# Performance work log

Measured on AMD Instinct MI355X. Metric: run time of the kernel, lower is better.

The kernel has to match this reference:

```python
import jax, jax.numpy as jnp
import numpy as np
from jax import lax

B, CIN, CV, H, W = 2, 256, 128, 96, 320
NS, K, PAD = 8, 3, 1
HID = 4 * CV
EPS = 1e-5

def _ffn_shapes(p):
    return {p+'_g': (CV,), p+'_b': (CV,), p+'_w1': (CV, HID), p+'_b1': (HID,),
            p+'_dw': (HID, 1, 3, 3), p+'_bdw': (HID,), p+'_w2': (HID, CV), p+'_b2': (CV,)}

def _win_shapes(p):
    return {p+'_g': (CV,), p+'_b': (CV,), p+'_wq': (CV, CV), p+'_wk': (CV, CV),
            p+'_wv': (CV, CV), p+'_wo': (CV, CV), p+'_bo': (CV,)}

PARAM_SHAPES = {'agg_w1': (CIN, CIN // 2), 'agg_b1': (CIN // 2,), 'agg_w2': (CIN // 2, CV), 'agg_b2': (CV,),
                'ol_g': (CV,), 'ol_b': (CV,), 'ol_wv': (CV, CV), 'ol_wa': (CV, K ** 4), 'ol_ba': (K ** 4,),
                'ol_wo': (CV, CV), 'ol_bo': (CV,)}
PARAM_SHAPES.update(_ffn_shapes('f1')); PARAM_SHAPES.update(_win_shapes('w'))
PARAM_SHAPES.update(_ffn_shapes('f2')); PARAM_SHAPES.update(_win_shapes('s'))
PARAM_SHAPES.update(_ffn_shapes('f3'))
PNAMES = list(PARAM_SHAPES.keys())


def ln(x, g, b):
    mu = x.mean(-1, keepdims=True)
    var = ((x - mu) ** 2).mean(-1, keepdims=True)
    return (x - mu) * lax.rsqrt(var + EPS) * g + b


def sink_softmax(logits):
    # softmax with an implicit extra zero-logit 'sink' slot (sink competition):
    # probs = exp(l) / (sum(exp(l)) + exp(0)), computed stably.
    m = jnp.maximum(logits.max(-1, keepdims=True), 0.0)
    e = jnp.exp(logits - m)
    return e / (e.sum(-1, keepdims=True) + jnp.exp(-m))


def outlook_attn(x, g, b, wv, wa, ba, wo, bo):
    # VOLO-style outlook attention, kernel K, stride 1, padding PAD (pool is identity at stride 1)
    Bb, Hh, Ww, C = x.shape
    xn = ln(x, g, b)
    v = xn @ wv                                                     # B,H,W,C
    vp = jnp.pad(v, ((0, 0), (PAD, PAD), (PAD, PAD), (0, 0)))
    patches = jnp.stack([vp[:, i:i + Hh, j:j + Ww, :] for i in range(K) for j in range(K)], axis=3)  # B,H,W,K*K,C
    attn = (xn @ wa + ba).reshape(Bb, Hh, Ww, K * K, K * K)
    attn = sink_softmax(attn)
    out = jnp.einsum('bhwpq,bhwqc->bhwpc', attn, patches)           # B,H,W,K*K,C
    acc = jnp.zeros_like(vp)                                        # fold (overlap-add)
    idx = 0
    for i in range(K):
        for j in range(K):
            acc = acc.at[:, i:i + Hh, j:j + Ww, :].add(out[:, :, :, idx, :])
            idx += 1
    y = acc[:, PAD:PAD + Hh, PAD:PAD + Ww, :]
    return y @ wo + bo


def swin_mask(Hh, Ww, wh, ww):
    # standard swin shifted-window cross-region mask, built statically
    sh, sw = wh // 2, ww // 2
    img = np.zeros((Hh, Ww), np.int32)
    cnt = 0
    for hs in (slice(0, -wh), slice(-wh, -sh), slice(-sh, None)):
        for ws in (slice(0, -ww), slice(-ww, -sw), slice(-sw, None)):
            img[hs, ws] = cnt; cnt += 1
    win = img.reshape(Hh // wh, wh, Ww // ww, ww).transpose(0, 2, 1, 3).reshape(-1, wh * ww)
    mask = np.where(win[:, :, None] != win[:, None, :], -100.0, 0.0).astype(np.float32)
    return jnp.asarray(mask)  # [NS*NS, L, L]


def window_attn(x, g, b, wq, wk, wv, wo, bo, with_shift):
    Bb, Hh, Ww, C = x.shape
    wh, ww = Hh // NS, Ww // NS
    xn = ln(x, g, b)
    if with_shift:
        xn = jnp.roll(xn, (-(wh // 2), -(ww // 2)), axis=(1, 2))

    def part(t):  # -> [B, NS*NS, wh*ww, C]
        return t.reshape(Bb, NS, wh, NS, ww, C).transpose(0, 1, 3, 2, 4, 5).reshape(Bb, NS * NS, wh * ww, C)

    q, k, v = part(xn @ wq), part(xn @ wk), part(xn @ wv)
    scores = jnp.einsum('bnqc,bnkc->bnqk', q, k) / jnp.sqrt(jnp.asarray(C, x.dtype))
    if with_shift:
        scores = scores + swin_mask(Hh, Ww, wh, ww)[None]
    out = jnp.einsum('bnqk,bnkc->bnqc', sink_softmax(scores), v)
    out = out.reshape(Bb, NS, NS, wh, ww, C).transpose(0, 1, 3, 2, 4, 5).reshape(Bb, Hh, Ww, C)
    if with_shift:
        out = jnp.roll(out, (wh // 2, ww // 2), axis=(1, 2))
    return out @ wo + bo


def conv_ffn(x, g, b, w1, b1, dw, bdw, w2, b2):
    # pre-norm conv FFN: 1x1 expand -> depthwise 3x3 -> GELU -> 1x1 project
    xn = ln(x, g, b)
    h = (xn @ w1 + b1).transpose(0, 3, 1, 2)                        # B,HID,H,W
    h = lax.conv_general_dilated(h, dw, (1, 1), 'SAME', feature_group_count=HID)
    h = h + bdw[None, :, None, None]
    h = jax.nn.gelu(h, approximate=False).transpose(0, 2, 3, 1)
    return h @ w2 + b2


def pos_embed(Bb, Hh, Ww, nf, dtype):
    # DETR-style normalized 2D sine/cosine positional embedding, nf feats per axis
    scale = 2.0 * np.pi
    eps = 1e-6
    ye = jnp.arange(1, Hh + 1, dtype=jnp.float32); ye = ye / (ye[-1] + eps) * scale
    xe = jnp.arange(1, Ww + 1, dtype=jnp.float32); xe = xe / (xe[-1] + eps) * scale
    dim_t = 10000.0 ** (2.0 * (jnp.arange(nf) // 2) / nf)

    def emb(p):  # [N] -> [N, nf]
        t = p[:, None] / dim_t
        return jnp.stack([jnp.sin(t[:, 0::2]), jnp.cos(t[:, 1::2])], axis=2).reshape(p.shape[0], -1)

    py, px = emb(ye), emb(xe)
    pos = jnp.concatenate([jnp.broadcast_to(py[:, None, :], (Hh, Ww, nf)),
                           jnp.broadcast_to(px[None, :, :], (Hh, Ww, nf))], axis=-1)
    return jnp.broadcast_to(pos[None], (Bb, Hh, Ww, 2 * nf)).astype(dtype)


def forward(x, p):
    f = x.transpose(0, 2, 3, 1)                                     # B,H,W,CIN
    f = jax.nn.relu(f @ p['agg_w1'] + p['agg_b1'])                  # channels_agg (BN folded, eval)
    f = f @ p['agg_w2'] + p['agg_b2']                               # B,H,W,CV
    f = f + outlook_attn(f, p['ol_g'], p['ol_b'], p['ol_wv'], p['ol_wa'], p['ol_ba'], p['ol_wo'], p['ol_bo'])
    f = f + conv_ffn(f, p['f1_g'], p['f1_b'], p['f1_w1'], p['f1_b1'], p['f1_dw'], p['f1_bdw'], p['f1_w2'], p['f1_b2'])
    f = f + pos_embed(f.shape[0], f.shape[1], f.shape[2], CV // 2, f.dtype)
    f = f + window_attn(f, p['w_g'], p['w_b'], p['w_wq'], p['w_wk'], p['w_wv'], p['w_wo'], p['w_bo'], False)
    f = f + conv_ffn(f, p['f2_g'], p['f2_b'], p['f2_w1'], p['f2_b1'], p['f2_dw'], p['f2_bdw'], p['f2_w2'], p['f2_b2'])
    f = f + window_attn(f, p['s_g'], p['s_b'], p['s_wq'], p['s_wk'], p['s_wv'], p['s_wo'], p['s_bo'], True)
    f = f + conv_ffn(f, p['f3_g'], p['f3_b'], p['f3_w1'], p['f3_b1'], p['f3_dw'], p['f3_bdw'], p['f3_w2'], p['f3_b2'])
    return f.transpose(0, 3, 1, 2)                                  # B,CV,H,W


def setup_inputs():
    keys = iter(jax.random.split(jax.random.key(0), 64))
    inp = {'x': jax.random.normal(next(keys), (B, CIN, H, W), jnp.float32)}
    for name, shp in PARAM_SHAPES.items():
        if name.endswith('_g'):
            inp[name] = jnp.ones(shp, jnp.float32)
        elif len(shp) == 1:
            inp[name] = jnp.zeros(shp, jnp.float32)
        else:
            inp[name] = jax.random.normal(next(keys), shp, jnp.float32) * 0.02
    return inp


def reference(x, agg_w1, agg_b1, agg_w2, agg_b2, ol_g, ol_b, ol_wv, ol_wa, ol_ba, ol_wo, ol_bo,
              f1_g, f1_b, f1_w1, f1_b1, f1_dw, f1_bdw, f1_w2, f1_b2,
              w_g, w_b, w_wq, w_wk, w_wv, w_wo, w_bo,
              f2_g, f2_b, f2_w1, f2_b1, f2_dw, f2_bdw, f2_w2, f2_b2,
              s_g, s_b, s_wq, s_wk, s_wv, s_wo, s_bo,
              f3_g, f3_b, f3_w1, f3_b1, f3_dw, f3_bdw, f3_w2, f3_b2):
    _l = locals()
    p = {k: _l[k] for k in PNAMES}
    return forward(x, p)
```

## Files before the change

kernel.cpp:

```cpp
#include <hip/hip_runtime.h>

typedef __bf16 bf16;
typedef __bf16 bf16x8 __attribute__((ext_vector_type(8)));
typedef __bf16 bf16x4 __attribute__((ext_vector_type(4)));
typedef float  f32x4  __attribute__((ext_vector_type(4)));

#define MFMA_BF16(a, b, c) __builtin_amdgcn_mfma_f32_16x16x32_bf16(a, b, c, 0, 0, 0)

constexpr int cB    = 2;
constexpr int cH    = 96;
constexpr int cW    = 320;
constexpr int cC    = 128;
constexpr int cNPIX = cH * cW;
constexpr int cNTOK = cB * cNPIX;
constexpr int cAS   = 84;

struct WJob  { const float* src; bf16* dst; int K; int M; };
struct WJobs { WJob j[19]; };

__global__ __launch_bounds__(256) void k_wt(WJobs jobs)
{
    __shared__ float tile[32][33];
    const WJob jb = jobs.j[blockIdx.z];
    int k0 = blockIdx.y * 32, m0 = blockIdx.x * 32;
    if (k0 >= jb.K || m0 >= jb.M) return;
    int tx = threadIdx.x, ty = threadIdx.y;
#pragma unroll
    for (int i = 0; i < 32; i += 8) {
        int kk = k0 + ty + i, mm = m0 + tx;
        tile[ty + i][tx] = (kk < jb.K && mm < jb.M) ? jb.src[(size_t)kk * jb.M + mm] : 0.f;
    }
    __syncthreads();
#pragma unroll
    for (int i = 0; i < 32; i += 8) {
        int mm = m0 + ty + i, kk = k0 + tx;
        if (mm < jb.M && kk < jb.K)
            jb.dst[(size_t)mm * jb.K + kk] = (bf16)tile[tx][ty + i];
    }
}

__global__ __launch_bounds__(256) void k_dwt(const float* s0, const float* s1, const float* s2,
                                             float* d0, float* d1, float* d2)
{
    const float* s = blockIdx.x == 0 ? s0 : (blockIdx.x == 1 ? s1 : s2);
    float*       d = blockIdx.x == 0 ? d0 : (blockIdx.x == 1 ? d1 : d2);
    for (int i = threadIdx.x; i < 512 * 9; i += 256) {
        int c = i / 9, tap = i - c * 9;
        d[tap * 512 + c] = s[i];
    }
}

__global__ __launch_bounds__(256) void k_postab(float* __restrict__ yt, float* __restrict__ xt)
{
    int i = blockIdx.x * 256 + threadIdx.x;
    const float TWO_PI = 6.283185307179586f;
    const float KSC = -9.210340371976184f / 32.f;
    if (i < 96 * 64) {
        int h = i >> 6, c = i & 63;
        float p = (float)(h + 1) * (TWO_PI / (96.f + 1e-6f));
        float val = p * expf((float)(c >> 1) * KSC);
        yt[i] = (c & 1) ? cosf(val) : sinf(val);
    }
    if (i < 320 * 64) {
        int w = i >> 6, c = i & 63;
        float p = (float)(w + 1) * (TWO_PI / (320.f + 1e-6f));
        float val = p * expf((float)(c >> 1) * KSC);
        xt[i] = (c & 1) ? cosf(val) : sinf(val);
    }
}

__global__ __launch_bounds__(256) void k_chw2hwc(const float* __restrict__ in,
                                                 bf16* __restrict__ out)
{
    __shared__ float tile[32][33];
    const int Cc = 256;
    int s0 = blockIdx.x * 32;
    int c0 = blockIdx.y * 32;
    int b  = blockIdx.z;
    const float* ip = in  + (size_t)b * Cc * cNPIX;
    bf16*        op = out + (size_t)b * cNPIX * Cc;
    int tx = threadIdx.x, ty = threadIdx.y;
#pragma unroll
    for (int i = 0; i < 32; i += 8)
        tile[ty + i][tx] = ip[(size_t)(c0 + ty + i) * cNPIX + s0 + tx];
    __syncthreads();
#pragma unroll
    for (int i = 0; i < 32; i += 8)
        op[(size_t)(s0 + ty + i) * Cc + c0 + tx] = (bf16)tile[tx][ty + i];
}

__global__ __launch_bounds__(256) void k_hwc2chw(const float* __restrict__ in,
                                                 float* __restrict__ out)
{
    __shared__ float tile[32][33];
    int s0 = blockIdx.x * 32;
    int c0 = blockIdx.y * 32;
    int b  = blockIdx.z;
    const float* ip = in  + (size_t)b * cNPIX * cC;
    float*       op = out + (size_t)b * cC * cNPIX;
    int tx = threadIdx.x, ty = threadIdx.y;
#pragma unroll
    for (int i = 0; i < 32; i += 8)
        tile[ty + i][tx] = ip[(size_t)(s0 + ty + i) * cC + c0 + tx];
    __syncthreads();
#pragma unroll
    for (int i = 0; i < 32; i += 8)
        op[(size_t)(c0 + ty + i) * cNPIX + s0 + tx] = tile[tx][ty + i];
}

template<int QKVS>
__global__ __launch_bounds__(256) void k_gemm128(const bf16* __restrict__ A,
                                                 const bf16* __restrict__ Wt,
                                                 const float* __restrict__ bias,
                                                 bf16* __restrict__ outB, int M,
                                                 bf16* __restrict__ vtb,
                                                 bf16* __restrict__ ksb)
{
    __shared__ bf16 As[128][136];
    __shared__ bf16 Sb[64][136];

    const int NS = M >> 7;
    const int l  = blockIdx.x;
    const int r8 = l % (8 * NS);
    const int qq = l / (8 * NS);
    const int bm = (qq * 8 + (r8 & 7)) * 128;
    const int bn = (r8 >> 3) * 128;

    const int t = threadIdx.x;
    const int lane = t & 63, wid = t >> 6;
    const int wm = (wid >> 1) * 64, wn = (wid & 1) * 64;
    const int lr = lane & 15, lg = lane >> 4;

    const bf16* wp = Wt + (size_t)(bn + wn + lr) * 128 + lg * 8;
    bf16x8 bwA[4], bwB[4];
#pragma unroll
    for (int nf = 0; nf < 4; ++nf)
        bwA[nf] = *(const bf16x8*)(wp + (size_t)(nf * 16) * 128);

#pragma unroll
    for (int i = 0; i < 8; ++i) {
        int o = i * 256 + t;
        int row = o >> 4, cg = (o & 15) * 8;
        *(bf16x8*)&As[row][cg] = *(const bf16x8*)(A + (size_t)(bm + row) * 128 + cg);
    }
    __syncthreads();

    const f32x4 zero4 = {0.f, 0.f, 0.f, 0.f};
    f32x4 acc[4][4];
#pragma unroll
    for (int i = 0; i < 4; ++i)
#pragma unroll
        for (int j = 0; j < 4; ++j) acc[i][j] = zero4;

#pragma unroll
    for (int ks = 0; ks < 4; ++ks) {
        const bf16x8* cur = (ks & 1) ? bwB : bwA;
        bf16x8*       nxt = (ks & 1) ? bwA : bwB;
        if (ks < 3) {
#pragma unroll
            for (int nf = 0; nf < 4; ++nf)
                nxt[nf] = *(const bf16x8*)(wp + (size_t)(nf * 16) * 128 + (ks + 1) * 32);
        }
        bf16x8 af[4];
#pragma unroll
        for (int mf = 0; mf < 4; ++mf)
            af[mf] = *(const bf16x8*)&As[wm + mf*16 + lr][ks*32 + lg*8];
        __builtin_amdgcn_s_setprio(1);
#pragma unroll
        for (int mf = 0; mf < 4; ++mf)
#pragma unroll
            for (int nf = 0; nf < 4; ++nf)
                acc[mf][nf] = MFMA_BF16(af[mf], cur[nf], acc[mf][nf]);
        __builtin_amdgcn_s_setprio(0);
    }

    const bool vpart = (QKVS >= 0) && (bn == 256);
    const bool kpart = (QKVS >= 0) && (bn == 128);
    if (!vpart) {
#pragma unroll
        for (int half = 0; half < 2; ++half) {
            __syncthreads();
            if ((wid >> 1) == half) {
#pragma unroll
                for (int nf = 0; nf < 4; ++nf) {
                    int col = wn + nf * 16 + lr;
                    float bv = bias ? bias[bn + col] : 0.f;
#pragma unroll
                    for (int mf = 0; mf < 4; ++mf)
#pragma unroll
                        for (int r = 0; r < 4; ++r)
                            Sb[mf * 16 + lg * 4 + r][col] = (bf16)(acc[mf][nf][r] + bv);
                }
            }
            __syncthreads();
            if (!kpart) {
                const int ldo = (QKVS >= 0) ? 128 : M;
#pragma unroll
                for (int i = 0; i < 4; ++i) {
                    int o = i * 256 + t;
                    int row = o >> 4, cg = (o & 15) * 8;
                    *(bf16x8*)(outB + (size_t)(bm + half * 64 + row) * ldo + bn + cg) =
                        *(const bf16x8*)&Sb[row][cg];
                }
            } else {
#pragma unroll
                for (int i = 0; i < 4; ++i) {
                    int o = i * 256 + t;
                    int row = o >> 4, cg = (o & 15) * 8;
                    int gt = bm + half * 64 + row;
                    int b_ = gt / cNPIX, hw = gt - b_ * cNPIX;
                    int h = hw / cW, w = hw - (hw / cW) * cW;
                    int h0 = (QKVS == 1) ? ((h + 90) % 96)  : h;
                    int w0 = (QKVS == 1) ? ((w + 300) % 320) : w;
                    int nh = h0 / 12, kh = h0 - nh * 12;
                    int nw = w0 / 40, kw = w0 - nw * 40;
                    size_t krow = (size_t)((b_ * 64 + nh * 8 + nw) * 480 + kh * 40 + kw);
                    *(bf16x8*)(ksb + krow * 128 + cg) = *(const bf16x8*)&Sb[row][cg];
                }
            }
        }
    } else {
        const int lr_ = t & 15, cg_ = t >> 4;
        const int gt = bm + lr_ * 8;
        const int b_ = gt / cNPIX, hw = gt % cNPIX;
        const int h = hw / cW, w = hw % cW;
        const int h0 = (QKVS == 1) ? ((h + 90) % 96) : h;
        const int nh = h0 / 12, kh = h0 - nh * 12;
#pragma unroll
        for (int cp = 0; cp < 2; ++cp) {
            __syncthreads();
            if ((wid & 1) == cp) {
#pragma unroll
                for (int nf = 0; nf < 4; ++nf) {
                    int cl = nf * 16 + lr;
#pragma unroll
                    for (int mf = 0; mf < 4; ++mf)
#pragma unroll
                        for (int r = 0; r < 4; ++r)
                            Sb[cl][wm + mf * 16 + lg * 4 + r] = (bf16)acc[mf][nf][r];
                }
            }
            __syncthreads();
#pragma unroll
            for (int i = 0; i < 4; ++i) {
                int chl = cg_ + 16 * i;
                int ch  = cp * 64 + chl;
                bf16x8 e = *(const bf16x8*)&Sb[chl][lr_ * 8];
#pragma unroll
                for (int hi = 0; hi < 2; ++hi) {
                    int wv = (QKVS == 1) ? ((w + hi * 4 + 300) % 320) : (w + hi * 4);
                    int nw = wv / 40, kw = wv - nw * 40;
                    bf16* dst = vtb + ((size_t)((b_ * 64 + nh * 8 + nw) * 128 + ch)) * 480 + kh * 40 + kw;
                    bf16x4 hv;
#pragma unroll
                    for (int j = 0; j < 4; ++j) hv[j] = e[hi * 4 + j];
                    *(bf16x4*)dst = hv;
                }
            }
        }
    }
}

__global__ __launch_bounds__(256) void k_gemm128_wa(const bf16* __restrict__ A,
                                                    const bf16* __restrict__ Wt,
                                                    const float* __restrict__ bias,
                                                    bf16* __restrict__ outA)
{
    __shared__ bf16 As[128][136];
    __shared__ bf16 Sb[64][88];

    const int bm = blockIdx.x * 128;
    const int t = threadIdx.x;
    const int lane = t & 63, wid = t >> 6;
    const int wm = (wid >> 1) * 64, wn = (wid & 1) * 64;
    const int lr = lane & 15, lg = lane >> 4;

    bf16x8 zrow;
#pragma unroll
    for (int j = 0; j < 8; ++j) zrow[j] = (bf16)0.f;

    bool okc[4];
    const bf16* wp = Wt + (size_t)(wn + lr) * 128 + lg * 8;
#pragma unroll
    for (int nf = 0; nf < 4; ++nf) okc[nf] = (wn + nf * 16 + lr) < 81;

    bf16x8 bwA[4], bwB[4];
#pragma unroll
    for (int nf = 0; nf < 4; ++nf)
        bwA[nf] = okc[nf] ? *(const bf16x8*)(wp + (size_t)(nf * 16) * 128) : zrow;

#pragma unroll
    for (int i = 0; i < 8; ++i) {
        int o = i * 256 + t;
        int row = o >> 4, cg = (o & 15) * 8;
        *(bf16x8*)&As[row][cg] = *(const bf16x8*)(A + (size_t)(bm + row) * 128 + cg);
    }
    __syncthreads();

    const f32x4 zero4 = {0.f, 0.f, 0.f, 0.f};
    f32x4 acc[4][4];
#pragma unroll
    for (int i = 0; i < 4; ++i)
#pragma unroll
        for (int j = 0; j < 4; ++j) acc[i][j] = zero4;

#pragma unroll
    for (int ks = 0; ks < 4; ++ks) {
        const bf16x8* cur = (ks & 1) ? bwB : bwA;
        bf16x8*       nxt = (ks & 1) ? bwA : bwB;
        if (ks < 3) {
#pragma unroll
            for (int nf = 0; nf < 4; ++nf)
                nxt[nf] = okc[nf] ? *(const bf16x8*)(wp + (size_t)(nf * 16) * 128 + (ks + 1) * 32) : zrow;
        }
        bf16x8 af[4];
#pragma unroll
        for (int mf = 0; mf < 4; ++mf)
            af[mf] = *(const bf16x8*)&As[wm + mf*16 + lr][ks*32 + lg*8];
        __builtin_amdgcn_s_setprio(1);
#pragma unroll
        for (int mf = 0; mf < 4; ++mf)
#pragma unroll
            for (int nf = 0; nf < 4; ++nf)
                acc[mf][nf] = MFMA_BF16(af[mf], cur[nf], acc[mf][nf]);
        __builtin_amdgcn_s_setprio(0);
    }

#pragma unroll
    for (int half = 0; half < 2; ++half) {
        __syncthreads();
        if ((wid >> 1) == half) {
#pragma unroll
            for (int nf = 0; nf < 4; ++nf) {
                int col = wn + nf * 16 + lr;
                if (col >= 84) continue;
                float bv = (col < 81) ? bias[col] : 0.f;
#pragma unroll
                for (int mf = 0; mf < 4; ++mf)
#pragma unroll
                    for (int r = 0; r < 4; ++r) {
                        float vv = (col < 81) ? (acc[mf][nf][r] + bv) : 0.f;
                        Sb[mf * 16 + lg * 4 + r][col] = (bf16)vv;
                    }
            }
        }
        __syncthreads();
#pragma unroll
        for (int i = 0; i < 6; ++i) {
            int o = i * 256 + t;
            if (o < 64 * 21) {
                int row = o / 21, cq = (o - row * 21) * 4;
                *(bf16x4*)(outA + (size_t)(bm + half * 64 + row) * cAS + cq) =
                    *(const bf16x4*)&Sb[row][cq];
            }
        }
    }
}

template<bool OUTBF, bool RELU, bool RES, bool POS, bool LNOUT>
__global__ __launch_bounds__(256) void k_gemm_res(const bf16* __restrict__ A,
                                                  const bf16* __restrict__ Wt,
                                                  const float* __restrict__ bias,
                                                  const float* __restrict__ res,
                                                  float* __restrict__ outF,
                                                  bf16* __restrict__ outB,
                                                  int K,
                                                  const float* __restrict__ ytab,
                                                  const float* __restrict__ xtab,
                                                  const float* __restrict__ lng,
                                                  const float* __restrict__ lnb,
                                                  bf16* __restrict__ xnbO)
{
    __shared__ bf16 As[128][40];
    __shared__ bf16 Bs[128][40];
    __shared__ float Sf[64][136];

    const int bm = blockIdx.x * 128;
    const int t = threadIdx.x;
    const int lane = t & 63, wid = t >> 6;
    const int wm = (wid >> 1) * 64, wn = (wid & 1) * 64;
    const int lr = lane & 15, lg = lane >> 4;

    const f32x4 zero4 = {0.f, 0.f, 0.f, 0.f};
    f32x4 acc[4][4];
#pragma unroll
    for (int i = 0; i < 4; ++i)
#pragma unroll
        for (int j = 0; j < 4; ++j) acc[i][j] = zero4;

    for (int k0 = 0; k0 < K; k0 += 32) {
#pragma unroll
        for (int i = 0; i < 2; ++i) {
            int idx = t + i * 256;
            int row = idx >> 2, kg = (idx & 3) * 8;
            *(bf16x8*)&As[row][kg] = *(const bf16x8*)(A + (size_t)(bm + row) * K + k0 + kg);
            *(bf16x8*)&Bs[row][kg] = *(const bf16x8*)(Wt + (size_t)row * K + k0 + kg);
        }
        __syncthreads();
        bf16x8 af[4], bf[4];
#pragma unroll
        for (int mf = 0; mf < 4; ++mf)
            af[mf] = *(const bf16x8*)&As[wm + mf*16 + lr][lg * 8];
#pragma unroll
        for (int nf = 0; nf < 4; ++nf)
            bf[nf] = *(const bf16x8*)&Bs[wn + nf*16 + lr][lg * 8];
        __builtin_amdgcn_s_setprio(1);
#pragma unroll
        for (int mf = 0; mf < 4; ++mf)
#pragma unroll
            for (int nf = 0; nf < 4; ++nf)
                acc[mf][nf] = MFMA_BF16(af[mf], bf[nf], acc[mf][nf]);
        __builtin_amdgcn_s_setprio(0);
        __syncthreads();
    }

    if (OUTBF) {
        bf16 (*Sb)[136] = (bf16(*)[136])Sf;
#pragma unroll
        for (int nf = 0; nf < 4; ++nf) {
            int col = wn + nf * 16 + lr;
            float bv = bias ? bias[col] : 0.f;
#pragma unroll
            for (int mf = 0; mf < 4; ++mf)
#pragma unroll
                for (int r = 0; r < 4; ++r) {
                    float vv = acc[mf][nf][r] + bv;
                    if (RELU) vv = fmaxf(vv, 0.f);
                    Sb[wm + mf * 16 + lg * 4 + r][col] = (bf16)vv;
                }
        }
        __syncthreads();
#pragma unroll
        for (int i = 0; i < 8; ++i) {
            int o = i * 256 + t;
            int row = o >> 4, cg = (o & 15) * 8;
            *(bf16x8*)(outB + (size_t)(bm + row) * 128 + cg) = *(const bf16x8*)&Sb[row][cg];
        }
    } else {
        for (int half = 0; half < 2; ++half) {
            __syncthreads();
            if ((wid >> 1) == half) {
#pragma unroll
                for (int nf = 0; nf < 4; ++nf) {
                    int col = wn + nf * 16 + lr;
                    float bv = bias ? bias[col] : 0.f;
#pragma unroll
                    for (int mf = 0; mf < 4; ++mf)
#pragma unroll
                        for (int r = 0; r < 4; ++r)
                            Sf[mf * 16 + lg * 4 + r][col] = acc[mf][nf][r] + bv;
                }
            }
            __syncthreads();
#pragma unroll
            for (int i = 0; i < 8; ++i) {
                int o = i * 256 + t;
                int row = o >> 5, cq = (o & 31) * 4;
                int grow = bm + half * 64 + row;
                float4 v = *(const float4*)&Sf[row][cq];
                if (POS) {
                    int hw = grow % cNPIX;
                    int h = hw / cW, w = hw - (hw / cW) * cW;
                    float4 p = (cq < 64) ? *(const float4*)(ytab + (h << 6) + cq)
                                         : *(const float4*)(xtab + (w << 6) + cq - 64);
                    v.x += p.x; v.y += p.y; v.z += p.z; v.w += p.w;
                }
                if (RES) {
                    float4 rr = *(const float4*)(res + (size_t)grow * 128 + cq);
                    v.x += rr.x; v.y += rr.y; v.z += rr.z; v.w += rr.w;
                }
                if (LNOUT) {
                    float s  = v.x + v.y + v.z + v.w;
                    float sq = v.x*v.x + v.y*v.y + v.z*v.z + v.w*v.w;
#pragma unroll
                    for (int mk = 1; mk < 32; mk <<= 1) {
                        s  += __shfl_xor(s,  mk);
                        sq += __shfl_xor(sq, mk);
                    }
                    float mu = s * (1.f / 128.f);
                    float rs = rsqrtf(sq * (1.f / 128.f) - mu * mu + 1e-5f);
                    float4 g4 = *(const float4*)(lng + cq);
                    float4 b4 = *(const float4*)(lnb + cq);
                    bf16x4 xo;
                    xo[0] = (bf16)((v.x - mu) * rs * g4.x + b4.x);
                    xo[1] = (bf16)((v.y - mu) * rs * g4.y + b4.y);
                    xo[2] = (bf16)((v.z - mu) * rs * g4.z + b4.z);
                    xo[3] = (bf16)((v.w - mu) * rs * g4.w + b4.w);
                    *(bf16x4*)(xnbO + (size_t)grow * 128 + cq) = xo;
                }
                *(float4*)(outF + (size_t)grow * 128 + cq) = v;
            }
        }
    }
}

__global__ __launch_bounds__(256) void k_olk_gather(const bf16* __restrict__ v,
                                                    const bf16* __restrict__ attn,
                                                    bf16* __restrict__ y)
{
    __shared__ float pr[16][84];
    __shared__ float coef[16][26];

    const int t  = threadIdx.x;
    const int px = t >> 4;
    const int j  = t & 15;
    const int pix = blockIdx.x * 16 + px;
    const int b  = pix / cNPIX;
    const int hw = pix % cNPIX;
    const int h = hw / cW, w = hw % cW;

    if (j < 9) {
        const int p  = j;
        const int pi = p / 3, pj = p - pi * 3;
        const int hh = h + 1 - pi, ww = w + 1 - pj;
        float prv[9];
        if ((unsigned)hh < (unsigned)cH && (unsigned)ww < (unsigned)cW) {
            const size_t row = (size_t)(b * cNPIX + hh * cW + ww);
            const bf16* arow = attn + row * cAS + p * 9;
            float lg[9];
            float m = 0.f;
#pragma unroll
            for (int q = 0; q < 9; ++q) { lg[q] = (float)arow[q]; m = fmaxf(m, lg[q]); }
            float se = 0.f;
#pragma unroll
            for (int q = 0; q < 9; ++q) { prv[q] = __expf(lg[q] - m); se += prv[q]; }
            float inv = 1.f / (se + __expf(-m));
#pragma unroll
            for (int q = 0; q < 9; ++q) prv[q] *= inv;
        } else {
#pragma unroll
            for (int q = 0; q < 9; ++q) prv[q] = 0.f;
        }
#pragma unroll
        for (int q = 0; q < 9; ++q) pr[px][p * 9 + q] = prv[q];
    }
    __syncthreads();

    for (int d = j; d < 25; d += 16) {
        const int a  = d / 5, bb = d - a * 5;
        float s = 0.f;
#pragma unroll
        for (int pi = 0; pi < 3; ++pi) {
            const int qi = pi + a - 2;
            if ((unsigned)qi >= 3u) continue;
#pragma unroll
            for (int pj = 0; pj < 3; ++pj) {
                const int qj = pj + bb - 2;
                if ((unsigned)qj >= 3u) continue;
                s += pr[px][(pi * 3 + pj) * 9 + qi * 3 + qj];
            }
        }
        coef[px][d] = s;
    }
    __syncthreads();

    float acc[8] = {};
    const size_t bbase = (size_t)b * cNPIX;
#pragma unroll
    for (int a = 0; a < 5; ++a) {
        const int sh = h + a - 2;
        if ((unsigned)sh >= (unsigned)cH) continue;
#pragma unroll
        for (int bb = 0; bb < 5; ++bb) {
            const int sw = w + bb - 2;
            if ((unsigned)sw >= (unsigned)cW) continue;
            const float cf = coef[px][a * 5 + bb];
            const bf16x8 v8 = *(const bf16x8*)(v + ((bbase + (size_t)sh * cW + sw) * 128 + j * 8));
#pragma unroll
            for (int e = 0; e < 8; ++e) acc[e] = fmaf(cf, (float)v8[e], acc[e]);
        }
    }
    bf16x8 o8;
#pragma unroll
    for (int e = 0; e < 8; ++e) o8[e] = (bf16)acc[e];
    *(bf16x8*)(y + (size_t)pix * 128 + j * 8) = o8;
}

__global__ __launch_bounds__(256) void k_dwconv_gelu(const bf16* __restrict__ h1,
                                                     const float* __restrict__ dwt,
                                                     const float* __restrict__ bdw,
                                                     bf16* __restrict__ h2)
{
    const int t   = threadIdx.x;
    const int c2  = t * 2;
    const int blk = blockIdx.x;
    const int row = blk >> 4;
    const int seg = blk & 15;
    const int bb  = row / cH, h = row % cH;
    const int w0  = seg * 20;

    float2 wgt[9];
#pragma unroll
    for (int k = 0; k < 9; ++k)
        wgt[k] = *(const float2*)(dwt + k * 512 + c2);
    if (h == 0) {
        wgt[0].x = wgt[0].y = wgt[1].x = wgt[1].y = wgt[2].x = wgt[2].y = 0.f;
    }
    if (h == cH - 1) {
        wgt[6].x = wgt[6].y = wgt[7].x = wgt[7].y = wgt[8].x = wgt[8].y = 0.f;
    }
    const float2 bias = *(const float2*)(bdw + c2);

    const size_t base = (size_t)bb * cNPIX;
    const int hm = (h == 0) ? 0 : h - 1;
    const int hp = (h == cH - 1) ? h : h + 1;
    const bf16* rp0 = h1 + (base + (size_t)hm * cW + w0) * 512 + c2;
    const bf16* rp1 = h1 + (base + (size_t)h  * cW + w0) * 512 + c2;
    const bf16* rp2 = h1 + (base + (size_t)hp * cW + w0) * 512 + c2;

    auto ldc = [&](const bf16* rp, int wofs) -> float2 {
        unsigned u = *(const unsigned*)(rp + (size_t)wofs * 512);
        float2 r;
        r.x = __uint_as_float(u << 16);
        r.y = __uint_as_float(u & 0xffff0000u);
        return r;
    };
    auto gelu = [](float x) -> float {
        float x2 = x * x;
        float z2 = fmaf(x2 * x, 0.0713548162726f, 1.5957691216057308f * x);
        float t1 = 1.f / (1.f + __expf(-z2));
        return x * t1;
    };

    float2 cm[3], c0[3], cp[3];
    if (seg == 0) {
#pragma unroll
        for (int r = 0; r < 3; ++r) { cm[r].x = 0.f; cm[r].y = 0.f; }
    } else {
        cm[0] = ldc(rp0, -1); cm[1] = ldc(rp1, -1); cm[2] = ldc(rp2, -1);
    }
    c0[0] = ldc(rp0, 0); c0[1] = ldc(rp1, 0); c0[2] = ldc(rp2, 0);

    bf16* op = h2 + (base + (size_t)h * cW + w0) * 512 + c2;

    for (int j = 0; j < 20; ++j) {
        if (j == 19 && seg == 15) {
#pragma unroll
            for (int r = 0; r < 3; ++r) { cp[r].x = 0.f; cp[r].y = 0.f; }
        } else {
            cp[0] = ldc(rp0, j + 1); cp[1] = ldc(rp1, j + 1); cp[2] = ldc(rp2, j + 1);
        }
        float a0 = bias.x, a1 = bias.y;
#pragma unroll
        for (int r = 0; r < 3; ++r) {
            a0 = fmaf(cm[r].x, wgt[r * 3 + 0].x, a0);
            a1 = fmaf(cm[r].y, wgt[r * 3 + 0].y, a1);
            a0 = fmaf(c0[r].x, wgt[r * 3 + 1].x, a0);
            a1 = fmaf(c0[r].y, wgt[r * 3 + 1].y, a1);
            a0 = fmaf(cp[r].x, wgt[r * 3 + 2].x, a0);
            a1 = fmaf(cp[r].y, wgt[r * 3 + 2].y, a1);
        }
        a0 = gelu(a0);
        a1 = gelu(a1);
        union { bf16 hh[2]; unsigned int u; } o2;
        o2.hh[0] = (bf16)a0;
        o2.hh[1] = (bf16)a1;
        *(unsigned int*)(op + (size_t)j * 512) = o2.u;
#pragma unroll
        for (int r = 0; r < 3; ++r) { cm[r] = c0[r]; c0[r] = cp[r]; }
    }
}

template<bool SHIFT>
__global__ __launch_bounds__(256) void k_win_attn(const bf16* __restrict__ q,
                                                  const bf16* __restrict__ ks,
                                                  const bf16* __restrict__ vt,
                                                  bf16* __restrict__ out)
{
    __shared__ bf16 Ks[32][136];
    __shared__ bf16 Vs[128][40];
    __shared__ bf16 Ps[4][16][44];

    const int t = threadIdx.x, lane = t & 63, wid = t >> 6;
    const int lr = lane & 15, lg = lane >> 4;
    const int wb = blockIdx.x;
    const int b  = wb >> 6, win = wb & 63;
    const int nh = win >> 3, nw = win & 7;
    const int qbase = blockIdx.y * 64 + wid * 16;

    const float SCALE   = 0.088388347648318447f;
    const float MASKRAW = 100.f / 0.088388347648318447f;

    auto tokOf = [&](int p) {
        int ph = nh * 12 + p / 40;
        int pw = nw * 40 + (p % 40);
        if (SHIFT) {
            ph += 6;  if (ph >= cH) ph -= cH;
            pw += 20; if (pw >= cW) pw -= cW;
        }
        return b * cNPIX + ph * cW + pw;
    };

    int qp = min(qbase + lr, 479);
    const bf16* qptr = q + (size_t)tokOf(qp) * 128;
    bf16x8 qf[4];
#pragma unroll
    for (int c = 0; c < 4; ++c)
        qf[c] = *(const bf16x8*)(qptr + c * 32 + lg * 8);

    int labq[4];
    if (SHIFT) {
#pragma unroll
        for (int r = 0; r < 4; ++r) {
            int qrow = min(qbase + lg * 4 + r, 479);
            int qr = qrow / 40, qc = qrow - qr * 40;
            int rh = (nh == 7) ? (qr < 6 ? 1 : 2) : 0;
            int rc = (nw == 7) ? (qc < 20 ? 1 : 2) : 0;
            labq[r] = rh * 3 + rc;
        }
    }

    const bf16* kbase = ks + (size_t)wb * 480 * 128;
    const bf16* vbase = vt + (size_t)wb * 128 * 480;
    auto loadK = [&](int kt, int i) {
        int idx = t + i * 256;
        int key = idx >> 4, cg = (idx & 15) * 8;
        return *(const bf16x8*)(kbase + (size_t)(kt * 32 + key) * 128 + cg);
    };
    auto loadV = [&](int kt, int i) {
        int idx = t + i * 256;
        int ch = idx >> 2, kq = (idx & 3) * 8;
        return *(const bf16x8*)(vbase + (size_t)ch * 480 + kt * 32 + kq);
    };

    bf16x8 kreg0 = loadK(0, 0), kreg1 = loadK(0, 1);
    bf16x8 vreg0 = loadV(0, 0), vreg1 = loadV(0, 1);

    int kc0 = lr, kr0 = 0;
    int kc1 = 16 + lr, kr1 = 0;

    const f32x4 zero4 = {0.f, 0.f, 0.f, 0.f};
    float m_run[4] = {0.f, 0.f, 0.f, 0.f};
    float mguard = 8.f;
    f32x4 l4 = zero4;
    f32x4 o[8];
#pragma unroll
    for (int nf = 0; nf < 8; ++nf) o[nf] = zero4;

    bf16x8 ones8;
#pragma unroll
    for (int j = 0; j < 8; ++j) ones8[j] = (bf16)1.f;

    for (int kt = 0; kt < 15; ++kt) {
        {
            int i0 = t, i1 = t + 256;
            *(bf16x8*)&Ks[i0 >> 4][(i0 & 15) * 8] = kreg0;
            *(bf16x8*)&Ks[i1 >> 4][(i1 & 15) * 8] = kreg1;
            *(bf16x8*)&Vs[i0 >> 2][(i0 & 3) * 8] = vreg0;
            *(bf16x8*)&Vs[i1 >> 2][(i1 & 3) * 8] = vreg1;
        }
        if (kt + 1 < 15) {
            kreg0 = loadK(kt + 1, 0); kreg1 = loadK(kt + 1, 1);
            vreg0 = loadV(kt + 1, 0); vreg1 = loadV(kt + 1, 1);
        }
        __syncthreads();

        f32x4 s0 = zero4, s1 = zero4;
        __builtin_amdgcn_s_setprio(1);
#pragma unroll
        for (int c = 0; c < 4; ++c) {
            bf16x8 kf0 = *(const bf16x8*)&Ks[lr][c * 32 + lg * 8];
            bf16x8 kf1 = *(const bf16x8*)&Ks[16 + lr][c * 32 + lg * 8];
            s0 = MFMA_BF16(qf[c], kf0, s0);
            s1 = MFMA_BF16(qf[c], kf1, s1);
        }
        __builtin_amdgcn_s_setprio(0);

        if (SHIFT) {
            int rh0 = (nh == 7) ? (kr0 < 6 ? 1 : 2) : 0;
            int rc0 = (nw == 7) ? (kc0 < 20 ? 1 : 2) : 0;
            int rh1 = (nh == 7) ? (kr1 < 6 ? 1 : 2) : 0;
            int rc1 = (nw == 7) ? (kc1 < 20 ? 1 : 2) : 0;
            int lab0 = rh0 * 3 + rc0;
            int lab1 = rh1 * 3 + rc1;
#pragma unroll
            for (int r = 0; r < 4; ++r) {
                if (labq[r] != lab0) s0[r] -= MASKRAW;
                if (labq[r] != lab1) s1[r] -= MASKRAW;
            }
        }
        kc0 += 32; if (kc0 >= 40) { kc0 -= 40; ++kr0; }
        kc1 += 32; if (kc1 >= 40) { kc1 -= 40; ++kr1; }

        float tm = fmaxf(fmaxf(fmaxf(s0[0], s0[1]), fmaxf(s0[2], s0[3])),
                         fmaxf(fmaxf(s1[0], s1[1]), fmaxf(s1[2], s1[3])));
#pragma unroll
        for (int off = 1; off < 16; off <<= 1) tm = fmaxf(tm, __shfl_xor(tm, off));
        if (tm * SCALE > mguard) {
#pragma unroll
            for (int r = 0; r < 4; ++r) {
                float mx = fmaxf(s0[r], s1[r]);
#pragma unroll
                for (int off = 1; off < 16; off <<= 1) mx = fmaxf(mx, __shfl_xor(mx, off));
                float nm = fmaxf(m_run[r], mx * SCALE);
                float sc = __expf(m_run[r] - nm);
#pragma unroll
                for (int nf = 0; nf < 8; ++nf) o[nf][r] *= sc;
                l4[r] *= sc;
                m_run[r] = nm;
            }
            mguard = fminf(fminf(m_run[0], m_run[1]), fminf(m_run[2], m_run[3])) + 8.f;
        }

#pragma unroll
        for (int r = 0; r < 4; ++r) {
            float p0 = __expf(fmaf(s0[r], SCALE, -m_run[r]));
            float p1 = __expf(fmaf(s1[r], SCALE, -m_run[r]));
            Ps[wid][lg * 4 + r][lr]      = (bf16)p0;
            Ps[wid][lg * 4 + r][16 + lr] = (bf16)p1;
        }

        bf16x8 pa = *(const bf16x8*)&Ps[wid][lr][lg * 8];
        __builtin_amdgcn_s_setprio(1);
        l4 = MFMA_BF16(pa, ones8, l4);
#pragma unroll
        for (int nf = 0; nf < 8; ++nf) {
            bf16x8 bv = *(const bf16x8*)&Vs[nf * 16 + lr][lg * 8];
            o[nf] = MFMA_BF16(pa, bv, o[nf]);
        }
        __builtin_amdgcn_s_setprio(0);
        __syncthreads();
    }

#pragma unroll
    for (int r = 0; r < 4; ++r) {
        int qrow = qbase + lg * 4 + r;
        if (qrow >= 480) continue;
        float inv = 1.f / (l4[r] + __expf(-m_run[r]));
        size_t ooff = (size_t)tokOf(qrow) * 128;
#pragma unroll
        for (int nf = 0; nf < 8; ++nf)
            out[ooff + nf * 16 + lr] = (bf16)(o[nf][r] * inv);
    }
}

extern "C" void kernel_launch(void* const* d_in, const int* in_sizes, int n_in,
                              void* d_out, int out_size, void* d_ws, size_t ws_size,
                              hipStream_t stream)
{
    (void)in_sizes; (void)n_in; (void)out_size; (void)ws_size;

    const float* X = (const float*)d_in[0];

    char* ws = (char*)d_ws;
    float* f    = (float*)ws;                                 ws += (size_t)cNTOK * 128 * 4;
    bf16*  xnb  = (bf16*)ws;                                  ws += (size_t)cNTOK * 128 * 2;
    bf16*  bufA = (bf16*)ws;                                  ws += (size_t)cNTOK * 512 * 2;
    bf16*  bufB = (bf16*)ws;                                  ws += (size_t)cNTOK * 512 * 2;
    bf16*  wts  = (bf16*)ws;

    size_t wo_off = 0;
    auto nextw = [&](int K, int M) { bf16* p = wts + wo_off; wo_off += (size_t)K * M; return p; };
    bf16* agg_w1t = nextw(256, 128);
    bf16* agg_w2t = nextw(128, 128);
    bf16* ol_wvt  = nextw(128, 128);
    bf16* ol_wat  = nextw(128, 81);
    bf16* ol_wot  = nextw(128, 128);
    bf16* f1_w1t  = nextw(128, 512);
    bf16* f1_w2t  = nextw(512, 128);
    bf16* w_qkvt  = nextw(128, 384);
    bf16* w_wot   = nextw(128, 128);
    bf16* f2_w1t  = nextw(128, 512);
    bf16* f2_w2t  = nextw(512, 128);
    bf16* s_qkvt  = nextw(128, 384);
    bf16* s_wot   = nextw(128, 128);
    bf16* f3_w1t  = nextw(128, 512);
    bf16* f3_w2t  = nextw(512, 128);
    float* dwt1 = (float*)(wts + wo_off);
    float* dwt2 = dwt1 + 512 * 9;
    float* dwt3 = dwt2 + 512 * 9;
    float* ytab = dwt3 + 512 * 9;
    float* xtab = ytab + 96 * 64;

    WJobs jobs;
    int ji = 0;
    auto addj = [&](int src_idx, bf16* dst, int K, int M) {
        jobs.j[ji++] = WJob{(const float*)d_in[src_idx], dst, K, M};
    };
    addj(1,  agg_w1t, 256, 128);
    addj(3,  agg_w2t, 128, 128);
    addj(7,  ol_wvt,  128, 128);
    addj(8,  ol_wat,  128, 81);
    addj(10, ol_wot,  128, 128);
    addj(14, f1_w1t,  128, 512);
    addj(18, f1_w2t,  512, 128);
    addj(22, w_qkvt,           128, 128);
    addj(23, w_qkvt + 128*128, 128, 128);
    addj(24, w_qkvt + 256*128, 128, 128);
    addj(25, w_wot,   128, 128);
    addj(29, f2_w1t,  128, 512);
    addj(33, f2_w2t,  512, 128);
    addj(37, s_qkvt,           128, 128);
    addj(38, s_qkvt + 128*128, 128, 128);
    addj(39, s_qkvt + 256*128, 128, 128);
    addj(40, s_wot,   128, 128);
    addj(44, f3_w1t,  128, 512);
    addj(48, f3_w2t,  512, 128);
    k_wt<<<dim3(16, 16, 19), dim3(32, 8), 0, stream>>>(jobs);
    k_dwt<<<3, 256, 0, stream>>>((const float*)d_in[16], (const float*)d_in[31],
                                 (const float*)d_in[46], dwt1, dwt2, dwt3);
    k_postab<<<80, 256, 0, stream>>>(ytab, xtab);

    const int nTT = cNTOK / 128;

    k_chw2hwc<<<dim3(cNPIX / 32, 256 / 32, cB), dim3(32, 8), 0, stream>>>(X, bufA);
    k_gemm_res<true, true, false, false, false><<<nTT, 256, 0, stream>>>(
        bufA, agg_w1t, (const float*)d_in[2], nullptr, nullptr, bufB, 256,
        nullptr, nullptr, nullptr, nullptr, nullptr);
    k_gemm_res<false, false, false, false, true><<<nTT, 256, 0, stream>>>(
        bufB, agg_w2t, (const float*)d_in[4], nullptr, f, nullptr, 128,
        nullptr, nullptr, (const float*)d_in[5], (const float*)d_in[6], xnb);

    {
        bf16*  vb   = bufA;
        bf16*  gout = bufA + (size_t)cNTOK * 128;
        bf16*  atn  = bufB;
        k_gemm128<-1><<<nTT, 256, 0, stream>>>(xnb, ol_wvt, nullptr, vb, 128, nullptr, nullptr);
        k_gemm128_wa<<<nTT, 256, 0, stream>>>(xnb, ol_wat, (const float*)d_in[9], atn);
        k_olk_gather<<<cNTOK / 16, 256, 0, stream>>>(vb, atn, gout);
        k_gemm_res<false, false, true, false, true><<<nTT, 256, 0, stream>>>(
            gout, ol_wot, (const float*)d_in[11], f, f, nullptr, 128,
            nullptr, nullptr, (const float*)d_in[12], (const float*)d_in[13], xnb);
    }

    auto run_ffn = [&](int base, bf16* w1t, bf16* w2t, float* dwt, bool pos,
                       const float* lnG, const float* lnB) {
        k_gemm128<-1><<<nTT * 4, 256, 0, stream>>>(
            xnb, w1t, (const float*)d_in[base + 3], bufA, 512, nullptr, nullptr);
        k_dwconv_gelu<<<cB * cH * 16, 256, 0, stream>>>(
            bufA, dwt, (const float*)d_in[base + 5], bufB);
        if (pos) {
            k_gemm_res<false, false, true, true, true><<<nTT, 256, 0, stream>>>(
                bufB, w2t, (const float*)d_in[base + 7], f, f, nullptr, 512,
                ytab, xtab, lnG, lnB, xnb);
        } else if (lnG) {
            k_gemm_res<false, false, true, false, true><<<nTT, 256, 0, stream>>>(
                bufB, w2t, (const float*)d_in[base + 7], f, f, nullptr, 512,
                nullptr, nullptr, lnG, lnB, xnb);
        } else {
            k_gemm_res<false, false, true, false, false><<<nTT, 256, 0, stream>>>(
                bufB, w2t, (const float*)d_in[base + 7], f, f, nullptr, 512,
                nullptr, nullptr, nullptr, nullptr, nullptr);
        }
    };

    auto run_win = [&](int base, bf16* qkvt, bf16* wot, bool shift,
                       const float* lnG, const float* lnB) {
        bf16* qb  = bufA;
        bf16* ksb = bufA + (size_t)cNTOK * 128;
        bf16* vtb = bufA + (size_t)cNTOK * 256;
        bf16* ao  = bufB;
        if (shift)
            k_gemm128<1><<<nTT * 3, 256, 0, stream>>>(xnb, qkvt, nullptr, qb, 384, vtb, ksb);
        else
            k_gemm128<0><<<nTT * 3, 256, 0, stream>>>(xnb, qkvt, nullptr, qb, 384, vtb, ksb);
        if (shift) k_win_attn<true ><<<dim3(128, 8), 256, 0, stream>>>(qb, ksb, vtb, ao);
        else       k_win_attn<false><<<dim3(128, 8), 256, 0, stream>>>(qb, ksb, vtb, ao);
        k_gemm_res<false, false, true, false, true><<<nTT, 256, 0, stream>>>(
            ao, wot, (const float*)d_in[base + 6], f, f, nullptr, 128,
            nullptr, nullptr, lnG, lnB, xnb);
    };

    run_ffn(12, f1_w1t, f1_w2t, dwt1, true,
            (const float*)d_in[20], (const float*)d_in[21]);
    run_win(20, w_qkvt, w_wot, false,
            (const float*)d_in[27], (const float*)d_in[28]);
    run_ffn(27, f2_w1t, f2_w2t, dwt2, false,
            (const float*)d_in[35], (const float*)d_in[36]);
    run_win(35, s_qkvt, s_wot, true,
            (const float*)d_in[42], (const float*)d_in[43]);
    run_ffn(42, f3_w1t, f3_w2t, dwt3, false, nullptr, nullptr);

    k_hwc2chw<<<dim3(cNPIX / 32, cC / 32, cB), dim3(32, 8), 0, stream>>>(f, (float*)d_out);
}
```

Measured before the change: 572.4 us.

## Load window-attention K/V fragments straight from global memory, dropping LDS staging

The window attention kernel no longer stages each 32-key K tile and V tile through shared memory with two block barriers per iteration. Each wave now loads its MFMA K and V fragments directly from global memory into registers, and the V loads are issued after the QK MFMAs so the score math can hide part of their latency. The 16-lane shuffle reduction that made the running-max guard uniform is also removed, so the rescale branch is now decided per lane. The costs are that the four waves each fetch the same K/V data (relying on cache), the next tile is no longer prefetched, and the per-lane branch together with the shuffles inside it risks diverging or inconsistent running maxima within a row.

```diff
diff --git a/kernel.cpp b/kernel.cpp
--- a/kernel.cpp
+++ b/kernel.cpp
@@ -667,8 +667,6 @@
                                                   const bf16* __restrict__ vt,
                                                   bf16* __restrict__ out)
 {
-    __shared__ bf16 Ks[32][136];
-    __shared__ bf16 Vs[128][40];
     __shared__ bf16 Ps[4][16][44];
 
     const int t = threadIdx.x, lane = t & 63, wid = t >> 6;
@@ -710,21 +708,8 @@
         }
     }
 
-    const bf16* kbase = ks + (size_t)wb * 480 * 128;
-    const bf16* vbase = vt + (size_t)wb * 128 * 480;
-    auto loadK = [&](int kt, int i) {
-        int idx = t + i * 256;
-        int key = idx >> 4, cg = (idx & 15) * 8;
-        return *(const bf16x8*)(kbase + (size_t)(kt * 32 + key) * 128 + cg);
-    };
-    auto loadV = [&](int kt, int i) {
-        int idx = t + i * 256;
-        int ch = idx >> 2, kq = (idx & 3) * 8;
-        return *(const bf16x8*)(vbase + (size_t)ch * 480 + kt * 32 + kq);
-    };
-
-    bf16x8 kreg0 = loadK(0, 0), kreg1 = loadK(0, 1);
-    bf16x8 vreg0 = loadV(0, 0), vreg1 = loadV(0, 1);
+    const bf16* kp0 = ks + (size_t)wb * 480 * 128 + (size_t)lr * 128 + lg * 8;
+    const bf16* vp  = vt + (size_t)wb * 128 * 480 + (size_t)lr * 480 + lg * 8;
 
     int kc0 = lr, kr0 = 0;
     int kc1 = 16 + lr, kr1 = 0;
@@ -742,29 +727,24 @@
     for (int j = 0; j < 8; ++j) ones8[j] = (bf16)1.f;
 
     for (int kt = 0; kt < 15; ++kt) {
-        {
-            int i0 = t, i1 = t + 256;
-            *(bf16x8*)&Ks[i0 >> 4][(i0 & 15) * 8] = kreg0;
-            *(bf16x8*)&Ks[i1 >> 4][(i1 & 15) * 8] = kreg1;
-            *(bf16x8*)&Vs[i0 >> 2][(i0 & 3) * 8] = vreg0;
-            *(bf16x8*)&Vs[i1 >> 2][(i1 & 3) * 8] = vreg1;
-        }
-        if (kt + 1 < 15) {
-            kreg0 = loadK(kt + 1, 0); kreg1 = loadK(kt + 1, 1);
-            vreg0 = loadV(kt + 1, 0); vreg1 = loadV(kt + 1, 1);
-        }
-        __syncthreads();
-
+        bf16x8 kv[8];
+#pragma unroll
+        for (int c = 0; c < 4; ++c) {
+            kv[c]     = *(const bf16x8*)(kp0 + (size_t)(kt * 32) * 128 + c * 32);
+            kv[4 + c] = *(const bf16x8*)(kp0 + (size_t)(kt * 32 + 16) * 128 + c * 32);
+        }
         f32x4 s0 = zero4, s1 = zero4;
         __builtin_amdgcn_s_setprio(1);
 #pragma unroll
         for (int c = 0; c < 4; ++c) {
-            bf16x8 kf0 = *(const bf16x8*)&Ks[lr][c * 32 + lg * 8];
-            bf16x8 kf1 = *(const bf16x8*)&Ks[16 + lr][c * 32 + lg * 8];
-            s0 = MFMA_BF16(qf[c], kf0, s0);
-            s1 = MFMA_BF16(qf[c], kf1, s1);
+            s0 = MFMA_BF16(qf[c], kv[c], s0);
+            s1 = MFMA_BF16(qf[c], kv[4 + c], s1);
         }
         __builtin_amdgcn_s_setprio(0);
+
+#pragma unroll
+        for (int nf = 0; nf < 8; ++nf)
+            kv[nf] = *(const bf16x8*)(vp + (size_t)(nf * 16) * 480 + kt * 32);
 
         if (SHIFT) {
             int rh0 = (nh == 7) ? (kr0 < 6 ? 1 : 2) : 0;
@@ -784,9 +764,7 @@
 
         float tm = fmaxf(fmaxf(fmaxf(s0[0], s0[1]), fmaxf(s0[2], s0[3])),
                          fmaxf(fmaxf(s1[0], s1[1]), fmaxf(s1[2], s1[3])));
-#pragma unroll
-        for (int off = 1; off < 16; off <<= 1) tm = fmaxf(tm, __shfl_xor(tm, off));
-        if (tm * SCALE > mguard) {
+        if (__builtin_expect(tm * SCALE > mguard, 0)) {
 #pragma unroll
             for (int r = 0; r < 4; ++r) {
                 float mx = fmaxf(s0[r], s1[r]);
@@ -814,12 +792,9 @@
         __builtin_amdgcn_s_setprio(1);
         l4 = MFMA_BF16(pa, ones8, l4);
 #pragma unroll
-        for (int nf = 0; nf < 8; ++nf) {
-            bf16x8 bv = *(const bf16x8*)&Vs[nf * 16 + lr][lg * 8];
-            o[nf] = MFMA_BF16(pa, bv, o[nf]);
-        }
+        for (int nf = 0; nf < 8; ++nf)
+            o[nf] = MFMA_BF16(pa, kv[nf], o[nf]);
         __builtin_amdgcn_s_setprio(0);
-        __syncthreads();
     }
 
 #pragma unroll
```

Result: slower. 657.0 us (+14.8%).
